# Kernel tuning notes

Measured on AMD Instinct MI355X. Metric: run time of the kernel, lower is better.

## Reference

```python
import jax, jax.numpy as jnp
import numpy as np

B, T, D = 2, 2048, 2048
H, HD = 16, 128            # num_heads, head_dim = D // H
DVH = 2                    # dynamic_value_num_heads
NVK = 4                    # num_v_keys = int(sqrt(H))
TOPK = DVH * 2             # = 4 <= NVK


def setup_inputs() -> dict:
    key = jax.random.key(0)
    ks = jax.random.split(key, 12)
    s = jnp.float32(0.02)
    return {
        "x": jax.random.normal(ks[0], (B, T, D), jnp.float32),
        "Wq": jax.random.normal(ks[1], (D, D), jnp.float32) * s,
        "bq": jnp.zeros((D,), jnp.float32),
        "Wk": jax.random.normal(ks[2], (D, D), jnp.float32) * s,
        "bk": jnp.zeros((D,), jnp.float32),
        "Wvq": jax.random.normal(ks[3], (HD * DVH, D), jnp.float32) * s,
        "bvq": jnp.zeros((HD * DVH,), jnp.float32),
        "v_keys": jax.random.normal(ks[4], (DVH, NVK, HD), jnp.float32) * s,
        "v_embed": jax.random.normal(ks[5], (H, HD * H), jnp.float32) * s,
        "Wo": jax.random.normal(ks[6], (D, D), jnp.float32) * s,
        "bo": jnp.zeros((D,), jnp.float32),
    }


def reference(x, Wq, bq, Wk, bk, Wvq, bvq, v_keys, v_embed, Wo, bo):
    b, t, d = x.shape
    # q/k projections -> [b, H, t, HD]
    q = (x @ Wq.T + bq).reshape(b, t, H, HD).transpose(0, 2, 1, 3)
    k = (x @ Wk.T + bk).reshape(b, t, H, HD).transpose(0, 2, 1, 3)

    # --- compute_value_states ---
    vq = (x @ Wvq.T + bvq).reshape(b, t, DVH, HD)          # [b,t,h,n]
    sim = jnp.einsum('bthn,hkn->bthk', vq, v_keys)         # [b,t,DVH,NVK]
    _, idx = jax.lax.top_k(sim, TOPK)                      # [b,t,DVH,TOPK]
    ve = v_embed[idx]                                      # gather -> [b,t,DVH,TOPK,d]
    # einsum 'btd,bthkd->btd' == x * sum over (h,k)
    vs = x * ve.sum(axis=(2, 3))                           # [b,t,d]
    v = vs.reshape(b, t, H, HD).transpose(0, 2, 1, 3)      # [b,H,t,HD]

    # --- hand-rolled causal attention ---
    scores = jnp.einsum('bhqd,bhkd->bhqk', q, k) / np.float32(np.sqrt(HD))
    min_val = jnp.finfo(x.dtype).min
    mask = jnp.triu(jnp.full((t, t), min_val, dtype=x.dtype), 1)
    scores = scores + mask
    w = jax.nn.softmax(scores.astype(jnp.float32), axis=-1).astype(x.dtype)
    o = jnp.einsum('bhqk,bhkd->bhqd', w, v)                # [b,H,t,HD]
    o = o.transpose(0, 2, 1, 3).reshape(b, t, d)
    return o @ Wo.T + bo
```

## Files before the change

kernel.cpp:

```cpp
#include <hip/hip_runtime.h>
#include <hip/hip_bf16.h>

#define DEV __device__ __forceinline__

typedef __bf16 bf16x8 __attribute__((ext_vector_type(8)));
typedef __bf16 bf16x4 __attribute__((ext_vector_type(4)));
typedef float f32x4 __attribute__((ext_vector_type(4)));

static constexpr int kB = 2, kT = 2048, kD = 2048, kH = 16, kHD = 128;
static constexpr int kBT = kB * kT;

#if __has_builtin(__builtin_amdgcn_exp2f)
DEV float fast_exp2(float x) { return __builtin_amdgcn_exp2f(x); }
#else
DEV float fast_exp2(float x) { return exp2f(x); }
#endif

DEV unsigned short f2bf(float f) {
  union { __hip_bfloat16 h; unsigned short u; } cv;
  cv.h = __float2bfloat16(f);
  return cv.u;
}

DEV void gl_lds16(const void* g, void* l) {
  __builtin_amdgcn_global_load_lds(
      (const __attribute__((address_space(1))) unsigned int*)g,
      (__attribute__((address_space(3))) unsigned int*)l, 16, 0, 0);
}

#define MFMA(a, b, c) __builtin_amdgcn_mfma_f32_16x16x32_bf16(a, b, c, 0, 0, 0)

DEV int swz4(int row) { return (row ^ (row >> 2)) & 3; }

__global__ __launch_bounds__(256) void prep_kernel(
    const float* __restrict__ x, const float* __restrict__ v_embed,
    const float* __restrict__ Wq, const float* __restrict__ Wk,
    const float* __restrict__ Wo, unsigned short* __restrict__ vt,
    unsigned short* __restrict__ xb, unsigned short* __restrict__ wqb,
    unsigned short* __restrict__ wkb, unsigned short* __restrict__ wob) {
  const int tid = threadIdx.x;
  const int bx = blockIdx.x;
  if (bx >= 1024) {
    const int j = bx - 1024;
    const int which = j >> 12;
    const int i = (j & 4095) * 256 + tid;
    const float* s = which == 0 ? Wq : which == 1 ? Wk : Wo;
    unsigned short* d = which == 0 ? wqb : which == 1 ? wkb : wob;
    float4 v = ((const float4*)s)[i];
    ushort4 o;
    o.x = f2bf(v.x); o.y = f2bf(v.y); o.z = f2bf(v.z); o.w = f2bf(v.w);
    ((ushort4*)d)[i] = o;
    return;
  }
  __shared__ __align__(16) unsigned short sT[128 * 72];
  const int t0 = (bx & 31) * 64, h = (bx >> 5) & 15, b = bx >> 9;
  const int d4 = tid & 31, r8 = tid >> 5;
  const int dg = h * kHD + d4 * 4;
  float4 e0 = *(const float4*)(v_embed + dg);
  float4 e1 = *(const float4*)(v_embed + kD + dg);
  float4 e2 = *(const float4*)(v_embed + 2 * kD + dg);
  float4 e3 = *(const float4*)(v_embed + 3 * kD + dg);
  float4 c4;
  c4.x = 2.f * (e0.x + e1.x + e2.x + e3.x);
  c4.y = 2.f * (e0.y + e1.y + e2.y + e3.y);
  c4.z = 2.f * (e0.z + e1.z + e2.z + e3.z);
  c4.w = 2.f * (e0.w + e1.w + e2.w + e3.w);
#pragma unroll
  for (int it = 0; it < 8; it++) {
    const int t = r8 + it * 8;
    const size_t row = (size_t)(b * kT + t0 + t) * kD + dg;
    float4 v = *(const float4*)(x + row);
    ushort4 xo;
    xo.x = f2bf(v.x); xo.y = f2bf(v.y); xo.z = f2bf(v.z); xo.w = f2bf(v.w);
    *(ushort4*)(xb + row) = xo;
    sT[(d4 * 4 + 0) * 72 + t] = f2bf(v.x * c4.x);
    sT[(d4 * 4 + 1) * 72 + t] = f2bf(v.y * c4.y);
    sT[(d4 * 4 + 2) * 72 + t] = f2bf(v.z * c4.z);
    sT[(d4 * 4 + 3) * 72 + t] = f2bf(v.w * c4.w);
  }
  __syncthreads();
#pragma unroll
  for (int it = 0; it < 4; it++) {
    const int hd = (tid >> 3) + it * 32;
    const int tt = (tid & 7) * 8;
    bf16x8 vv = *(const bf16x8*)(sT + hd * 72 + tt);
    *(bf16x8*)(vt + ((size_t)((b * kH + h) * kHD + hd)) * kT + t0 + tt) = vv;
  }
}

__global__ __launch_bounds__(512, 2) void gemm8p_qk(
    const unsigned short* __restrict__ A, const unsigned short* __restrict__ B1,
    const unsigned short* __restrict__ B2, const float* __restrict__ bias1,
    const float* __restrict__ bias2, unsigned short* __restrict__ C1,
    unsigned short* __restrict__ C2, float scale1, float scale2) {
  constexpr int N = kD, K = kD;
  constexpr int NT = K / 32;
  __shared__ __align__(16) unsigned short As[4][256 * 32];
  __shared__ __align__(16) unsigned short Bs[4][256 * 32];
  const int lb = blockIdx.x + (blockIdx.y << 3) + (blockIdx.z << 7);
  const int xcd = lb & 7, r2 = lb >> 3;
  const int bzn = xcd & 1;
  const int byn = ((xcd >> 1) << 2) + (r2 >> 3);
  const int bxn = r2 & 7;
  const unsigned short* Bm = bzn ? B2 : B1;
  const float* bias = bzn ? bias2 : bias1;
  unsigned short* Cout = bzn ? C2 : C1;
  const float scale = bzn ? scale2 : scale1;

  const int tid = threadIdx.x;
  const int lane = tid & 63, wave = tid >> 6;
  const int wr = wave >> 2, wc = wave & 3;
  const int m0 = byn * 256, n0 = bxn * 256;
  const int frow = lane & 15, fc = lane >> 4;

  f32x4 acc[8][4];
#pragma unroll
  for (int i = 0; i < 8; i++)
#pragma unroll
    for (int j = 0; j < 4; j++)
#pragma unroll
      for (int r = 0; r < 4; r++) acc[i][j][r] = 0.f;

  const int q0 = tid, q1 = tid + 512;
  const int r0 = q0 >> 2, c0 = (q0 & 3) ^ swz4(r0);
  const int r1 = q1 >> 2, c1 = (q1 & 3) ^ swz4(r1);

  const unsigned short* Ab = A + (size_t)m0 * K;
  const unsigned short* Bb = Bm + (size_t)n0 * K;

  auto stA = [&](int bf, int k0) {
    gl_lds16(Ab + (size_t)r0 * K + k0 + c0 * 8, &As[bf][q0 * 8]);
    gl_lds16(Ab + (size_t)r1 * K + k0 + c1 * 8, &As[bf][q1 * 8]);
  };
  auto stB = [&](int bf, int k0) {
    gl_lds16(Bb + (size_t)r0 * K + k0 + c0 * 8, &Bs[bf][q0 * 8]);
    gl_lds16(Bb + (size_t)r1 * K + k0 + c1 * 8, &Bs[bf][q1 * 8]);
  };

  stA(0, 0); stB(0, 0);
  stA(1, 32); stB(1, 32);
  stA(2, 64); stB(2, 64);
  asm volatile("s_waitcnt vmcnt(8)" ::: "memory");
  __builtin_amdgcn_s_barrier();
  __builtin_amdgcn_sched_barrier(0);

  for (int k = 0; k < NT; ++k) {
    const int buf = k & 3;
    const int nbuf = (k + 3) & 3;
    const int kn = (k + 3) * 32;
    const bool pre = (k + 3) < NT;
    const unsigned short* Asb = As[buf];
    const unsigned short* Bsb = Bs[buf];

    bf16x8 bfr[4], af[4];
#pragma unroll
    for (int ni = 0; ni < 4; ni++) {
      const int row = wc * 64 + ni * 16 + frow;
      bfr[ni] = *(const bf16x8*)(Bsb + (row * 4 + (fc ^ swz4(row))) * 8);
    }
#pragma unroll
    for (int mi = 0; mi < 4; mi++) {
      const int row = wr * 128 + mi * 16 + frow;
      af[mi] = *(const bf16x8*)(Asb + (row * 4 + (fc ^ swz4(row))) * 8);
    }
    if (pre) stA(nbuf, kn);
    __builtin_amdgcn_s_barrier();
    asm volatile("s_waitcnt lgkmcnt(0)" ::: "memory");
    __builtin_amdgcn_sched_barrier(0);
    __builtin_amdgcn_s_setprio(1);
#pragma unroll
    for (int mi = 0; mi < 4; mi++)
#pragma unroll
      for (int ni = 0; ni < 4; ni++)
        acc[mi][ni] = MFMA(af[mi], bfr[ni], acc[mi][ni]);
    __builtin_amdgcn_s_setprio(0);
    __builtin_amdgcn_s_barrier();
    __builtin_amdgcn_sched_barrier(0);

    bf16x8 af2[4];
#pragma unroll
    for (int mi = 0; mi < 4; mi++) {
      const int row = wr * 128 + (mi + 4) * 16 + frow;
      af2[mi] = *(const bf16x8*)(Asb + (row * 4 + (fc ^ swz4(row))) * 8);
    }
    if (pre) stB(nbuf, kn);
    if (k < NT - 3)
      asm volatile("s_waitcnt vmcnt(8)" ::: "memory");
    else if (k == NT - 3)
      asm volatile("s_waitcnt vmcnt(4)" ::: "memory");
    else if (k == NT - 2)
      asm volatile("s_waitcnt vmcnt(0)" ::: "memory");
    __builtin_amdgcn_s_barrier();
    asm volatile("s_waitcnt lgkmcnt(0)" ::: "memory");
    __builtin_amdgcn_sched_barrier(0);
    __builtin_amdgcn_s_setprio(1);
#pragma unroll
    for (int mi = 0; mi < 4; mi++)
#pragma unroll
      for (int ni = 0; ni < 4; ni++)
        acc[mi + 4][ni] = MFMA(af2[mi], bfr[ni], acc[mi + 4][ni]);
    __builtin_amdgcn_s_setprio(0);
    __builtin_amdgcn_s_barrier();
    __builtin_amdgcn_sched_barrier(0);
  }

#pragma unroll
  for (int ni = 0; ni < 4; ni++) {
    const int n = n0 + wc * 64 + ni * 16 + frow;
    const float bs = bias[n];
#pragma unroll
    for (int mi = 0; mi < 8; mi++) {
      const int mb = m0 + wr * 128 + mi * 16 + fc * 4;
#pragma unroll
      for (int r = 0; r < 4; r++) {
        const float v = (acc[mi][ni][r] + bs) * scale;
        Cout[(size_t)(mb + r) * N + n] = f2bf(v);
      }
    }
  }
}

template <int NREP, bool BF16OUT, bool FUSED2>
__global__ __launch_bounds__(256, 4) void gemm_bt(
    const unsigned short* __restrict__ A, const unsigned short* __restrict__ B1,
    const unsigned short* __restrict__ B2, const float* __restrict__ bias1,
    const float* __restrict__ bias2, void* __restrict__ C1, void* __restrict__ C2,
    float scale1, float scale2) {
  constexpr int BN = NREP * 32;
  constexpr int N = kD, K = kD;
  __shared__ __align__(16) unsigned short As[2][128 * 32], Bs[2][BN * 32];
  int bxn, byn, bzn;
  if constexpr (FUSED2) {
    const int lb = blockIdx.x + (blockIdx.y << 4) + (blockIdx.z << 9);
    const int xcd = lb & 7, r = lb >> 3;
    bzn = xcd & 1;
    bxn = (((xcd >> 1) & 1) << 3) + (r & 7);
    byn = ((xcd >> 2) << 4) + (r >> 3);
  } else {
    const int lb = blockIdx.x + (blockIdx.y << 4);
    const int xcd = lb & 7, r = lb >> 3;
    bzn = 0;
    bxn = ((xcd & 1) << 3) + (r & 7);
    byn = ((xcd >> 1) << 3) + (r >> 3);
  }
  const unsigned short* Bm = (FUSED2 && bzn) ? B2 : B1;
  const float* bias = (FUSED2 && bzn) ? bias2 : bias1;
  void* Cout = (FUSED2 && bzn) ? C2 : C1;
  const float scale = (FUSED2 && bzn) ? scale2 : scale1;
  const int tid = threadIdx.x;
  const int lane = tid & 63, wave = tid >> 6;
  const int wr = wave >> 1, wc = wave & 1;
  const int m0 = byn * 128, n0 = bxn * BN;
  const int frow = lane & 15, fc = lane >> 4;

  f32x4 acc[4][NREP];
#pragma unroll
  for (int i = 0; i < 4; i++)
#pragma unroll
    for (int j = 0; j < NREP; j++)
#pragma unroll
      for (int r = 0; r < 4; r++) acc[i][j][r] = 0.f;

  const int r0 = tid >> 2, c0 = (tid & 3) ^ swz4(r0);
  const int p1 = tid + 256;
  const int r1 = p1 >> 2, c1 = (p1 & 3) ^ swz4(r1);

  const unsigned short* Ab = A + (size_t)m0 * K;
  const unsigned short* Bb = Bm + (size_t)n0 * K;

  for (int k0 = 0; k0 < K; k0 += 64) {
    __syncthreads();
#pragma unroll
    for (int hh = 0; hh < 2; hh++) {
      const int kk = k0 + hh * 32;
      gl_lds16(Ab + (size_t)r0 * K + kk + c0 * 8, &As[hh][tid * 8]);
      gl_lds16(Ab + (size_t)r1 * K + kk + c1 * 8, &As[hh][p1 * 8]);
      gl_lds16(Bb + (size_t)r0 * K + kk + c0 * 8, &Bs[hh][tid * 8]);
      if constexpr (NREP == 4)
        gl_lds16(Bb + (size_t)r1 * K + kk + c1 * 8, &Bs[hh][p1 * 8]);
    }
    __syncthreads();
#pragma unroll
    for (int hh = 0; hh < 2; hh++) {
      bf16x8 af[4], bfr[NREP];
#pragma unroll
      for (int mi = 0; mi < 4; mi++) {
        int row = wr * 64 + mi * 16 + frow;
        af[mi] = *(const bf16x8*)(&As[hh][(row * 4 + (fc ^ swz4(row))) * 8]);
      }
#pragma unroll
      for (int ni = 0; ni < NREP; ni++) {
        int row = wc * (NREP * 16) + ni * 16 + frow;
        bfr[ni] = *(const bf16x8*)(&Bs[hh][(row * 4 + (fc ^ swz4(row))) * 8]);
      }
#pragma unroll
      for (int mi = 0; mi < 4; mi++)
#pragma unroll
        for (int ni = 0; ni < NREP; ni++)
          acc[mi][ni] = MFMA(af[mi], bfr[ni], acc[mi][ni]);
    }
  }
#pragma unroll
  for (int ni = 0; ni < NREP; ni++) {
    const int n = n0 + wc * (NREP * 16) + ni * 16 + frow;
    const float bs = bias[n];
#pragma unroll
    for (int mi = 0; mi < 4; mi++) {
      const int mb = m0 + wr * 64 + mi * 16 + fc * 4;
#pragma unroll
      for (int r = 0; r < 4; r++) {
        const float v = (acc[mi][ni][r] + bs) * scale;
        if (BF16OUT)
          ((unsigned short*)Cout)[(size_t)(mb + r) * N + n] = f2bf(v);
        else
          ((float*)Cout)[(size_t)(mb + r) * N + n] = v;
      }
    }
  }
}

__global__ __launch_bounds__(256, 2) void attn2_kernel(
    const unsigned short* __restrict__ Q, const unsigned short* __restrict__ Kg,
    const unsigned short* __restrict__ Vt, unsigned short* __restrict__ O) {
  __shared__ __align__(16) unsigned short sK[2][64 * 128];
  __shared__ __align__(16) unsigned short sV[2][64 * 128];
  const int tid = threadIdx.x, l = tid & 63, w = tid >> 6;
  const int g = l >> 4, q15 = l & 15;
  const int bid = blockIdx.x;
  const int xcd = bid & 7, rest = bid >> 3;
  const int gidx = xcd + 8 * (rest & 3);
  const int pi = rest >> 2;
  const int h = gidx & 15, b = gidx >> 4;

  for (int half = 0; half < 2; half++) {
    const int qt = half == 0 ? (31 - pi) : pi;
    const int q0 = qt * 64;
    const int nkb = qt + 1;
    const int q = q0 + w * 16 + q15;

    __syncthreads();
    for (int i = 0; i < 4; i++) {
      const int idx = tid + i * 256;
      const int key = idx >> 4, cc = (idx & 15) ^ (key & 15);
      gl_lds16(Kg + (size_t)(b * kT + key) * kD + h * kHD + cc * 8,
               &sK[0][idx * 8]);
    }
    for (int i = 0; i < 4; i++) {
      const int idx = tid + i * 256;
      const int hd = idx >> 3;
      const int cc = (idx & 7) ^ (hd & 7) ^ (((hd >> 3) & 1) << 2);
      gl_lds16(Vt + ((size_t)((b * kH + h) * kHD + hd)) * kT + cc * 8,
               &sV[0][idx * 8]);
    }

    bf16x8 qf[4];
    const unsigned short* Qrow = Q + (size_t)(b * kT + q) * kD + h * kHD;
#pragma unroll
    for (int kk = 0; kk < 4; kk++)
      qf[kk] = *(const bf16x8*)(Qrow + kk * 32 + g * 8);

    f32x4 oacc[8];
#pragma unroll
    for (int ni = 0; ni < 8; ni++)
      for (int r = 0; r < 4; r++) oacc[ni][r] = 0.f;
    float m_i = -1e30f, l_i = 0.f;

    for (int kb = 0; kb < nkb; kb++) {
      const int bb = kb & 1;
      __syncthreads();
      if (kb + 1 < nkb) {
        const int k0n = (kb + 1) * 64;
        const int nb = 1 - bb;
#pragma unroll
        for (int i = 0; i < 4; i++) {
          const int idx = tid + i * 256;
          const int key = idx >> 4, cc = (idx & 15) ^ (key & 15);
          gl_lds16(Kg + (size_t)(b * kT + k0n + key) * kD + h * kHD + cc * 8,
                   &sK[nb][idx * 8]);
        }
#pragma unroll
        for (int i = 0; i < 4; i++) {
          const int idx = tid + i * 256;
          const int hd = idx >> 3;
          const int cc = (idx & 7) ^ (hd & 7) ^ (((hd >> 3) & 1) << 2);
          gl_lds16(Vt + ((size_t)((b * kH + h) * kHD + hd)) * kT + k0n + cc * 8,
                   &sV[nb][idx * 8]);
        }
      }

      f32x4 st[4];
#pragma unroll
      for (int s = 0; s < 4; s++)
        for (int r = 0; r < 4; r++) st[s][r] = 0.f;
#pragma unroll
      for (int s = 0; s < 4; s++) {
        const int key = s * 16 + q15;
#pragma unroll
        for (int kk = 0; kk < 4; kk++) {
          bf16x8 kf = *(const bf16x8*)(
              &sK[bb][(key * 16 + ((kk * 4 + g) ^ (key & 15))) * 8]);
          st[s] = MFMA(kf, qf[kk], st[s]);
        }
      }
      if (kb == nkb - 1) {
        const int k0 = kb * 64;
#pragma unroll
        for (int s = 0; s < 4; s++)
          for (int r = 0; r < 4; r++)
            if (k0 + s * 16 + g * 4 + r > q) st[s][r] = -1e30f;
      }
      float mx = -1e30f;
#pragma unroll
      for (int s = 0; s < 4; s++)
        for (int r = 0; r < 4; r++) mx = fmaxf(mx, st[s][r]);
      const bool defer = __all(mx - m_i <= 8.0f);
      float mn, alpha;
      if (defer) {
        mn = m_i;
        alpha = 1.f;
      } else {
        mx = fmaxf(mx, __shfl_xor(mx, 16, 64));
        mx = fmaxf(mx, __shfl_xor(mx, 32, 64));
        mn = fmaxf(m_i, mx);
        alpha = fast_exp2(m_i - mn);
      }
      float rs = 0.f;
      union { bf16x8 v; unsigned short u[8]; } pkv[2];
#pragma unroll
      for (int s = 0; s < 4; s++)
        for (int r = 0; r < 4; r++) {
          const float p = fast_exp2(st[s][r] - mn);
          rs += p;
          pkv[s >> 1].u[(s & 1) * 4 + r] = f2bf(p);
        }
      rs += __shfl_xor(rs, 16, 64);
      rs += __shfl_xor(rs, 32, 64);
      m_i = mn;
      l_i = l_i * alpha + rs;
      if (!defer) {
#pragma unroll
        for (int ni = 0; ni < 8; ni++)
          for (int r = 0; r < 4; r++) oacc[ni][r] *= alpha;
      }
#pragma unroll
      for (int ni = 0; ni < 8; ni++) {
        const int hd = ni * 16 + q15;
        const int hx = (hd & 7) ^ (((hd >> 3) & 1) << 2), base = hd * 8;
#pragma unroll
        for (int c = 0; c < 2; c++) {
          const int c4l = 8 * c + g;
          const int c4h = 8 * c + 4 + g;
          bf16x4 lo = *(const bf16x4*)(
              &sV[bb][(base + ((c4l >> 1) ^ hx)) * 8 + (c4l & 1) * 4]);
          bf16x4 hi = *(const bf16x4*)(
              &sV[bb][(base + ((c4h >> 1) ^ hx)) * 8 + (c4h & 1) * 4]);
          bf16x8 vf = __builtin_shufflevector(lo, hi, 0, 1, 2, 3, 4, 5, 6, 7);
          oacc[ni] = MFMA(vf, pkv[c].v, oacc[ni]);
        }
      }
    }
    const float inv = 1.f / l_i;
    unsigned short* Orow = O + (size_t)(b * kT + q) * kD + h * kHD;
#pragma unroll
    for (int ni = 0; ni < 8; ni++) {
      ushort4 o4;
      o4.x = f2bf(oacc[ni][0] * inv);
      o4.y = f2bf(oacc[ni][1] * inv);
      o4.z = f2bf(oacc[ni][2] * inv);
      o4.w = f2bf(oacc[ni][3] * inv);
      *(ushort4*)(Orow + ni * 16 + g * 4) = o4;
    }
  }
}

extern "C" void kernel_launch(void* const* d_in, const int* in_sizes, int n_in,
                              void* d_out, int out_size, void* d_ws, size_t ws_size,
                              hipStream_t stream) {
  const float* x       = (const float*)d_in[0];
  const float* Wq      = (const float*)d_in[1];
  const float* bq      = (const float*)d_in[2];
  const float* Wk      = (const float*)d_in[3];
  const float* bk      = (const float*)d_in[4];
  const float* v_embed = (const float*)d_in[8];
  const float* Wo      = (const float*)d_in[9];
  const float* bo      = (const float*)d_in[10];
  float* out = (float*)d_out;

  char* w = (char*)d_ws;
  unsigned short* xb  = (unsigned short*)w; w += (size_t)kBT * kD * 2;
  unsigned short* qb  = (unsigned short*)w; w += (size_t)kBT * kD * 2;
  unsigned short* kb  = (unsigned short*)w; w += (size_t)kBT * kD * 2;
  unsigned short* ob  = (unsigned short*)w; w += (size_t)kBT * kD * 2;
  unsigned short* vtb = (unsigned short*)w; w += (size_t)kBT * kD * 2;
  unsigned short* wqb = (unsigned short*)w; w += (size_t)kD * kD * 2;
  unsigned short* wkb = (unsigned short*)w; w += (size_t)kD * kD * 2;
  unsigned short* wob = (unsigned short*)w; w += (size_t)kD * kD * 2;

  prep_kernel<<<dim3(1024 + 3 * 4096), 256, 0, stream>>>(
      x, v_embed, Wq, Wk, Wo, vtb, xb, wqb, wkb, wob);

  const float scaleQ = 0.08838834764831845f * 1.4426950408889634f;
  gemm8p_qk<<<dim3(kD / 256, kBT / 256, 2), 512, 0, stream>>>(
      xb, wqb, wkb, bq, bk, qb, kb, scaleQ, 1.0f);

  attn2_kernel<<<dim3(512), 256, 0, stream>>>(qb, kb, vtb, ob);

  gemm_bt<4, false, false><<<dim3(kD / 128, kBT / 128, 1), 256, 0, stream>>>(
      ob, wob, nullptr, bo, nullptr, out, nullptr, 1.0f, 1.0f);
}
```

Before: 308.8 us.

## Replace output projection GEMM with 512-thread 4-stage pipelined kernel

```diff
diff --git a/kernel.cpp b/kernel.cpp
--- a/kernel.cpp
+++ b/kernel.cpp
@@ -220,101 +220,103 @@
   }
 }
 
-template <int NREP, bool BF16OUT, bool FUSED2>
-__global__ __launch_bounds__(256, 4) void gemm_bt(
-    const unsigned short* __restrict__ A, const unsigned short* __restrict__ B1,
-    const unsigned short* __restrict__ B2, const float* __restrict__ bias1,
-    const float* __restrict__ bias2, void* __restrict__ C1, void* __restrict__ C2,
-    float scale1, float scale2) {
-  constexpr int BN = NREP * 32;
+__global__ __launch_bounds__(512, 2) void gemm8p_o(
+    const unsigned short* __restrict__ A, const unsigned short* __restrict__ B,
+    const float* __restrict__ bias, float* __restrict__ C) {
   constexpr int N = kD, K = kD;
-  __shared__ __align__(16) unsigned short As[2][128 * 32], Bs[2][BN * 32];
-  int bxn, byn, bzn;
-  if constexpr (FUSED2) {
-    const int lb = blockIdx.x + (blockIdx.y << 4) + (blockIdx.z << 9);
-    const int xcd = lb & 7, r = lb >> 3;
-    bzn = xcd & 1;
-    bxn = (((xcd >> 1) & 1) << 3) + (r & 7);
-    byn = ((xcd >> 2) << 4) + (r >> 3);
-  } else {
-    const int lb = blockIdx.x + (blockIdx.y << 4);
-    const int xcd = lb & 7, r = lb >> 3;
-    bzn = 0;
-    bxn = ((xcd & 1) << 3) + (r & 7);
-    byn = ((xcd >> 1) << 3) + (r >> 3);
-  }
-  const unsigned short* Bm = (FUSED2 && bzn) ? B2 : B1;
-  const float* bias = (FUSED2 && bzn) ? bias2 : bias1;
-  void* Cout = (FUSED2 && bzn) ? C2 : C1;
-  const float scale = (FUSED2 && bzn) ? scale2 : scale1;
+  constexpr int NT = K / 32;
+  __shared__ __align__(16) unsigned short As[4][128 * 32];
+  __shared__ __align__(16) unsigned short Bs[4][256 * 32];
+  const int lb = blockIdx.x + (blockIdx.y << 3);
+  const int xcd = lb & 7, r2 = lb >> 3;
+  const int byn = ((xcd >> 1) << 3) + (r2 >> 2);
+  const int bxn = ((xcd & 1) << 2) + (r2 & 3);
+
   const int tid = threadIdx.x;
   const int lane = tid & 63, wave = tid >> 6;
-  const int wr = wave >> 1, wc = wave & 1;
-  const int m0 = byn * 128, n0 = bxn * BN;
+  const int wr = wave >> 2, wc = wave & 3;
+  const int m0 = byn * 128, n0 = bxn * 256;
   const int frow = lane & 15, fc = lane >> 4;
 
-  f32x4 acc[4][NREP];
+  f32x4 acc[4][4];
 #pragma unroll
   for (int i = 0; i < 4; i++)
 #pragma unroll
-    for (int j = 0; j < NREP; j++)
+    for (int j = 0; j < 4; j++)
 #pragma unroll
       for (int r = 0; r < 4; r++) acc[i][j][r] = 0.f;
 
-  const int r0 = tid >> 2, c0 = (tid & 3) ^ swz4(r0);
-  const int p1 = tid + 256;
-  const int r1 = p1 >> 2, c1 = (p1 & 3) ^ swz4(r1);
+  const int rA = tid >> 2, cA = (tid & 3) ^ swz4(rA);
+  const int q0 = tid, q1 = tid + 512;
+  const int rB0 = q0 >> 2, cB0 = (q0 & 3) ^ swz4(rB0);
+  const int rB1 = q1 >> 2, cB1 = (q1 & 3) ^ swz4(rB1);
 
   const unsigned short* Ab = A + (size_t)m0 * K;
-  const unsigned short* Bb = Bm + (size_t)n0 * K;
-
-  for (int k0 = 0; k0 < K; k0 += 64) {
-    __syncthreads();
-#pragma unroll
-    for (int hh = 0; hh < 2; hh++) {
-      const int kk = k0 + hh * 32;
-      gl_lds16(Ab + (size_t)r0 * K + kk + c0 * 8, &As[hh][tid * 8]);
-      gl_lds16(Ab + (size_t)r1 * K + kk + c1 * 8, &As[hh][p1 * 8]);
-      gl_lds16(Bb + (size_t)r0 * K + kk + c0 * 8, &Bs[hh][tid * 8]);
-      if constexpr (NREP == 4)
-        gl_lds16(Bb + (size_t)r1 * K + kk + c1 * 8, &Bs[hh][p1 * 8]);
-    }
-    __syncthreads();
-#pragma unroll
-    for (int hh = 0; hh < 2; hh++) {
-      bf16x8 af[4], bfr[NREP];
-#pragma unroll
-      for (int mi = 0; mi < 4; mi++) {
-        int row = wr * 64 + mi * 16 + frow;
-        af[mi] = *(const bf16x8*)(&As[hh][(row * 4 + (fc ^ swz4(row))) * 8]);
-      }
-#pragma unroll
-      for (int ni = 0; ni < NREP; ni++) {
-        int row = wc * (NREP * 16) + ni * 16 + frow;
-        bfr[ni] = *(const bf16x8*)(&Bs[hh][(row * 4 + (fc ^ swz4(row))) * 8]);
-      }
-#pragma unroll
-      for (int mi = 0; mi < 4; mi++)
-#pragma unroll
-        for (int ni = 0; ni < NREP; ni++)
-          acc[mi][ni] = MFMA(af[mi], bfr[ni], acc[mi][ni]);
-    }
-  }
-#pragma unroll
-  for (int ni = 0; ni < NREP; ni++) {
-    const int n = n0 + wc * (NREP * 16) + ni * 16 + frow;
+  const unsigned short* Bb = B + (size_t)n0 * K;
+
+  auto stage = [&](int bf, int k0) {
+    gl_lds16(Ab + (size_t)rA * K + k0 + cA * 8, &As[bf][tid * 8]);
+    gl_lds16(Bb + (size_t)rB0 * K + k0 + cB0 * 8, &Bs[bf][q0 * 8]);
+    gl_lds16(Bb + (size_t)rB1 * K + k0 + cB1 * 8, &Bs[bf][q1 * 8]);
+  };
+
+  stage(0, 0);
+  stage(1, 32);
+  stage(2, 64);
+  asm volatile("s_waitcnt vmcnt(6)" ::: "memory");
+  __builtin_amdgcn_s_barrier();
+  __builtin_amdgcn_sched_barrier(0);
+
+  for (int k = 0; k < NT; ++k) {
+    const int buf = k & 3;
+    const int nbuf = (k + 3) & 3;
+    const int kn = (k + 3) * 32;
+    const bool pre = (k + 3) < NT;
+    const unsigned short* Asb = As[buf];
+    const unsigned short* Bsb = Bs[buf];
+
+    bf16x8 af[4], bfr[4];
+#pragma unroll
+    for (int mi = 0; mi < 4; mi++) {
+      const int row = wr * 64 + mi * 16 + frow;
+      af[mi] = *(const bf16x8*)(Asb + (row * 4 + (fc ^ swz4(row))) * 8);
+    }
+#pragma unroll
+    for (int ni = 0; ni < 4; ni++) {
+      const int row = wc * 64 + ni * 16 + frow;
+      bfr[ni] = *(const bf16x8*)(Bsb + (row * 4 + (fc ^ swz4(row))) * 8);
+    }
+    if (pre) stage(nbuf, kn);
+    if (k < NT - 3)
+      asm volatile("s_waitcnt vmcnt(6)" ::: "memory");
+    else if (k == NT - 3)
+      asm volatile("s_waitcnt vmcnt(3)" ::: "memory");
+    else if (k == NT - 2)
+      asm volatile("s_waitcnt vmcnt(0)" ::: "memory");
+    __builtin_amdgcn_s_barrier();
+    asm volatile("s_waitcnt lgkmcnt(0)" ::: "memory");
+    __builtin_amdgcn_sched_barrier(0);
+    __builtin_amdgcn_s_setprio(1);
+#pragma unroll
+    for (int mi = 0; mi < 4; mi++)
+#pragma unroll
+      for (int ni = 0; ni < 4; ni++)
+        acc[mi][ni] = MFMA(af[mi], bfr[ni], acc[mi][ni]);
+    __builtin_amdgcn_s_setprio(0);
+    __builtin_amdgcn_s_barrier();
+    __builtin_amdgcn_sched_barrier(0);
+  }
+
+#pragma unroll
+  for (int ni = 0; ni < 4; ni++) {
+    const int n = n0 + wc * 64 + ni * 16 + frow;
     const float bs = bias[n];
 #pragma unroll
     for (int mi = 0; mi < 4; mi++) {
       const int mb = m0 + wr * 64 + mi * 16 + fc * 4;
 #pragma unroll
-      for (int r = 0; r < 4; r++) {
-        const float v = (acc[mi][ni][r] + bs) * scale;
-        if (BF16OUT)
-          ((unsigned short*)Cout)[(size_t)(mb + r) * N + n] = f2bf(v);
-        else
-          ((float*)Cout)[(size_t)(mb + r) * N + n] = v;
-      }
+      for (int r = 0; r < 4; r++)
+        C[(size_t)(mb + r) * N + n] = acc[mi][ni][r] + bs;
     }
   }
 }
@@ -505,6 +507,5 @@
 
   attn2_kernel<<<dim3(512), 256, 0, stream>>>(qb, kb, vtb, ob);
 
-  gemm_bt<4, false, false><<<dim3(kD / 128, kBT / 128, 1), 256, 0, stream>>>(
-      ob, wob, nullptr, bo, nullptr, out, nullptr, 1.0f, 1.0f);
-}
+  gemm8p_o<<<dim3(kD / 256, kBT / 128), 512, 0, stream>>>(ob, wob, bo, out);
+}
```

Result: no change. 310.8 us (+0.6%).
